# Performance work log

Hardware: AMD Instinct MI355X
Metric: run time of the kernel (lower is better)

Reference implementation:

```python
import jax, jax.numpy as jnp
import numpy as np

CH_IN, CH_OUT, KH, KW = 64, 128, 3, 3


def setup_inputs() -> dict:
    key = jax.random.key(0)
    k1, k2, k3 = jax.random.split(key, 3)
    x = jax.random.normal(k1, (16, CH_IN, 256, 256), dtype=jnp.float32)
    W_hat = jax.random.normal(k2, (CH_OUT, CH_IN * KH * KW), dtype=jnp.float32)
    M_hat = jax.random.normal(k3, (CH_OUT, CH_IN * KH * KW), dtype=jnp.float32)
    return {"x": x, "W_hat": W_hat, "M_hat": M_hat}


def reference(x, W_hat, M_hat):
    # NAC weight transform, then a standard same-padded conv (no bias).
    # Patch flattening order in the original (narrow(-1)/narrow(-2) then reshape)
    # matches (C_in, KH, KW) conv weight layout.
    W = jnp.tanh(W_hat) * jax.nn.sigmoid(M_hat)          # [C_out, C_in*KH*KW]
    W = W.reshape(CH_OUT, CH_IN, KH, KW)                  # OIHW
    out = jax.lax.conv_general_dilated(
        x, W,
        window_strides=(1, 1),
        padding=((KH // 2, KH // 2), (KW // 2, KW // 2)),
        dimension_numbers=("NCHW", "OIHW", "NCHW"),
    )
    return out
```

## Files before the change

### kernel.cpp

```cpp
#include <hip/hip_runtime.h>
#include <hip/hip_bf16.h>
#include <stdint.h>


#define CH_IN  64
#define CH_OUT 128
#define HW     256

typedef __attribute__((ext_vector_type(8))) short short8;
typedef __attribute__((ext_vector_type(4))) float f32x4;

#define AF_BYTES 147456u
#define ZP_BYTE  147456u
#define XB_BYTE  147712u
#define WS_NEED  (147712ull + 134217728ull)

static __device__ __forceinline__ uint32_t pack_bf16(float a, float b) {
    uint32_t ua = __builtin_bit_cast(uint32_t, a);
    uint32_t ub = __builtin_bit_cast(uint32_t, b);
    ua = (ua + 0x7FFFu + ((ua >> 16) & 1u)) >> 16;
    ub = (ub + 0x7FFFu + ((ub >> 16) & 1u));
    return (ua & 0xFFFFu) | (ub & 0xFFFF0000u);
}

__global__ void __launch_bounds__(256) nac_prep(const float* __restrict__ Wh,
                                                const float* __restrict__ Mh,
                                                uint32_t* __restrict__ ws32) {
    if (blockIdx.x == 0 && threadIdx.x < 64) ws32[ZP_BYTE / 4 + threadIdx.x] = 0;

    int f = blockIdx.x * 256 + threadIdx.x;
    if (f >= 9 * 8 * 2 * 64) return;
    int lane = f & 63;
    int s    = (f >> 6) & 1;
    int ms   = (f >> 7) & 7;
    int t    = f >> 10;
    int co   = ms * 16 + (lane & 15);
    int ci0  = s * 32 + ((lane >> 4) << 3);

    uint32_t pk[4];
#pragma unroll
    for (int j2 = 0; j2 < 4; ++j2) {
        int ci = ci0 + 2 * j2;
        int k0 = ci * 9 + t;
        int k1 = k0 + 9;
        float w0 = tanhf(Wh[co * 576 + k0]);
        float m0 = Mh[co * 576 + k0];
        float w1 = tanhf(Wh[co * 576 + k1]);
        float m1 = Mh[co * 576 + k1];
        float v0 = w0 * (1.0f / (1.0f + expf(-m0)));
        float v1 = w1 * (1.0f / (1.0f + expf(-m1)));
        pk[j2] = pack_bf16(v0, v1);
    }
    int fragidx = ((t * 8 + ms) * 2 + s) * 64 + lane;
    reinterpret_cast<uint4*>(ws32)[fragidx] = make_uint4(pk[0], pk[1], pk[2], pk[3]);
}

__global__ void __launch_bounds__(256) nac_convert(const float* __restrict__ x,
                                                   uint32_t* __restrict__ xb) {
    int bid = blockIdx.x;
    int h   = bid & 255;
    int n   = bid >> 8;
    int px  = threadIdx.x;
    const float* xr = x + ((size_t)n * CH_IN * HW + h) * HW + px;
    uint32_t* orow = xb + ((size_t)(n * HW + h) * HW + px) * 32;
#pragma unroll
    for (int g = 0; g < 8; ++g) {
        float v0 = xr[(size_t)(g * 8 + 0) * HW * HW];
        float v1 = xr[(size_t)(g * 8 + 1) * HW * HW];
        float v2 = xr[(size_t)(g * 8 + 2) * HW * HW];
        float v3 = xr[(size_t)(g * 8 + 3) * HW * HW];
        float v4 = xr[(size_t)(g * 8 + 4) * HW * HW];
        float v5 = xr[(size_t)(g * 8 + 5) * HW * HW];
        float v6 = xr[(size_t)(g * 8 + 6) * HW * HW];
        float v7 = xr[(size_t)(g * 8 + 7) * HW * HW];
        uint4 wd;
        wd.x = pack_bf16(v0, v1); wd.y = pack_bf16(v2, v3);
        wd.z = pack_bf16(v4, v5); wd.w = pack_bf16(v6, v7);
        *reinterpret_cast<uint4*>(orow + g * 4) = wd;
    }
}

__global__ void __launch_bounds__(256)
nac_conv2(const uint32_t* __restrict__ xb, const uint32_t* __restrict__ Af,
          float* __restrict__ out, const uint32_t* __restrict__ zp) {
    __shared__ __align__(1024) uint32_t xl[2112 * 4];

    unsigned bid = blockIdx.x;
    unsigned idx = (bid & 7u) * 1024u + (bid >> 3);
    int ht = idx & 127;
    int wt = (idx >> 7) & 3;
    int n  = idx >> 9;
    int h0 = ht * 2;
    int w0 = wt * 64;

    int tid = threadIdx.x;
    int g   = tid & 7;
    int q   = tid >> 3;

#pragma unroll
    for (int it = 0; it < 9; ++it) {
        if (it < 8 || tid < 64) {
            const int rp = it * 32 + q;
            const int r0 = (it * 32) / 66;
            const int r  = (rp >= (r0 + 1) * 66) ? r0 + 1 : r0;
            const int p  = rp - r * 66;
            const int hh = h0 - 1 + r;
            const int ww = w0 - 1 + p;
            const bool valid = ((unsigned)hh < 256u) & ((unsigned)ww < 256u);
            const uint32_t* src = valid
                ? xb + ((size_t)((n * 256 + hh) * 256 + ww) * 32 + ((g ^ (p & 7)) << 2))
                : zp;
            __builtin_amdgcn_global_load_lds(
                (const __attribute__((address_space(1))) uint32_t*)src,
                (__attribute__((address_space(3))) uint32_t*)&xl[(it * 256 + (tid & ~63)) * 4],
                16, 0, 0);
        }
    }
    __syncthreads();

    int lane = tid & 63;
    int wv   = tid >> 6;
    int wm   = wv >> 1;
    int wn   = wv & 1;
    int col  = lane & 15;
    int row4 = lane >> 4;

    int bcol[2][3];
#pragma unroll
    for (int s = 0; s < 2; ++s)
#pragma unroll
        for (int kw = 0; kw < 3; ++kw)
            bcol[s][kw] = (col + kw) * 128 +
                          ((((s * 4) + row4) ^ ((col + kw) & 7)) * 16);

    f32x4 acc[4][4];
#pragma unroll
    for (int mi = 0; mi < 4; ++mi)
#pragma unroll
        for (int ni = 0; ni < 4; ++ni) acc[mi][ni] = (f32x4){0.f, 0.f, 0.f, 0.f};

    const short8* Afr = reinterpret_cast<const short8*>(Af);
    const char* lb = reinterpret_cast<const char*>(xl);

#pragma unroll
    for (int t = 0; t < 9; ++t) {
        const int kh = t / 3, kw = t % 3;
        short8 a[2][4];
#pragma unroll
        for (int s = 0; s < 2; ++s)
#pragma unroll
            for (int mi = 0; mi < 4; ++mi)
                a[s][mi] = Afr[((t * 8 + (wm * 4 + mi)) * 2 + s) * 64 + lane];
#pragma unroll
        for (int s = 0; s < 2; ++s) {
#pragma unroll
            for (int ni = 0; ni < 4; ++ni) {
                short8 b = *reinterpret_cast<const short8*>(
                    lb + ((wn + kh) * 66 + ni * 16) * 128 + bcol[s][kw]);
#pragma unroll
                for (int mi = 0; mi < 4; ++mi)
                    acc[mi][ni] = __builtin_amdgcn_mfma_f32_16x16x32_bf16(
                        a[s][mi], b, acc[mi][ni], 0, 0, 0);
            }
        }
    }

#pragma unroll
    for (int mi = 0; mi < 4; ++mi) {
#pragma unroll
        for (int reg = 0; reg < 4; ++reg) {
            int co = wm * 64 + mi * 16 + row4 * 4 + reg;
            float* op = out + (((size_t)n * CH_OUT + co) * HW + (h0 + wn)) * HW + w0;
#pragma unroll
            for (int ni = 0; ni < 4; ++ni) op[ni * 16 + col] = acc[mi][ni][reg];
        }
    }
}

__global__ void __launch_bounds__(256) nac_conv_fb(const float* __restrict__ x,
                                                   const uint32_t* __restrict__ Af,
                                                   float* __restrict__ out) {
    __shared__ uint32_t xl[8 * 272 * 4];

    unsigned bid = blockIdx.x;
    unsigned idx = (bid & 7u) * 1024u + (bid >> 3);
    int ht = idx & 127;
    int wt = (idx >> 7) & 3;
    int n  = idx >> 9;
    int h0 = ht * 2;
    int w0 = wt * 64;
    int tid = threadIdx.x;

    const float* xn = x + (size_t)n * CH_IN * HW * HW;
    for (int it = 0; it < 9; ++it) {
        int task = tid + it * 256;
        if (task < 2176) {
            int r   = task / 544;
            int rem = task - r * 544;
            int pg  = rem / 68;
            int c   = rem - pg * 68;
            int hrow = h0 - 1 + r;
            int w    = w0 - 1 + c;
            float v[8];
            if ((unsigned)hrow < 256u && (unsigned)w < 256u) {
                const float* p = xn + ((size_t)(pg * 8) * HW + hrow) * HW + w;
#pragma unroll
                for (int e = 0; e < 8; ++e) v[e] = p[(size_t)e * HW * HW];
            } else {
#pragma unroll
                for (int e = 0; e < 8; ++e) v[e] = 0.0f;
            }
            uint4 wd;
            wd.x = pack_bf16(v[0], v[1]);
            wd.y = pack_bf16(v[2], v[3]);
            wd.z = pack_bf16(v[4], v[5]);
            wd.w = pack_bf16(v[6], v[7]);
            *reinterpret_cast<uint4*>(&xl[(pg * 272 + r * 68 + c) * 4]) = wd;
        }
    }
    __syncthreads();

    int lane = tid & 63;
    int wv   = tid >> 6;
    int wm   = wv >> 1;
    int wn   = wv & 1;
    int row4 = lane >> 4;
    int col  = lane & 15;

    f32x4 acc[4][4];
#pragma unroll
    for (int mi = 0; mi < 4; ++mi)
#pragma unroll
        for (int ni = 0; ni < 4; ++ni) acc[mi][ni] = (f32x4){0.f, 0.f, 0.f, 0.f};

    const short8* Afr = reinterpret_cast<const short8*>(Af);
    for (int t = 0; t < 9; ++t) {
        int kh = t / 3, kw = t % 3;
        short8 a[2][4];
#pragma unroll
        for (int s = 0; s < 2; ++s)
#pragma unroll
            for (int mi = 0; mi < 4; ++mi)
                a[s][mi] = Afr[((t * 8 + (wm * 4 + mi)) * 2 + s) * 64 + lane];
#pragma unroll
        for (int s = 0; s < 2; ++s) {
            short8 b[4];
#pragma unroll
            for (int ni = 0; ni < 4; ++ni) {
                int pg = s * 4 + row4;
                int pp = (wn + kh) * 68 + ni * 16 + col + kw;
                b[ni] = *reinterpret_cast<const short8*>(&xl[(pg * 272 + pp) * 4]);
            }
#pragma unroll
            for (int mi = 0; mi < 4; ++mi)
#pragma unroll
                for (int ni = 0; ni < 4; ++ni)
                    acc[mi][ni] = __builtin_amdgcn_mfma_f32_16x16x32_bf16(
                        a[s][mi], b[ni], acc[mi][ni], 0, 0, 0);
        }
    }

#pragma unroll
    for (int mi = 0; mi < 4; ++mi) {
#pragma unroll
        for (int reg = 0; reg < 4; ++reg) {
            int co = wm * 64 + mi * 16 + row4 * 4 + reg;
            float* op = out + (((size_t)n * CH_OUT + co) * HW + (h0 + wn)) * HW + w0;
#pragma unroll
            for (int ni = 0; ni < 4; ++ni) op[ni * 16 + col] = acc[mi][ni][reg];
        }
    }
}

extern "C" void kernel_launch(void* const* d_in, const int* in_sizes, int n_in,
                              void* d_out, int out_size, void* d_ws, size_t ws_size,
                              hipStream_t stream) {
    const float* x  = (const float*)d_in[0];
    const float* Wh = (const float*)d_in[1];
    const float* Mh = (const float*)d_in[2];
    float* out = (float*)d_out;
    uint32_t* ws32 = (uint32_t*)d_ws;
    const uint32_t* Af = ws32;
    const uint32_t* zp = ws32 + ZP_BYTE / 4;
    uint32_t* xb = ws32 + XB_BYTE / 4;

    nac_prep<<<36, 256, 0, stream>>>(Wh, Mh, ws32);
    if (ws_size >= WS_NEED) {
        nac_convert<<<4096, 256, 0, stream>>>(x, xb);
        nac_conv2<<<8192, 256, 0, stream>>>(xb, Af, out, zp);
    } else {
        nac_conv_fb<<<8192, 256, 0, stream>>>(x, Af, out);
    }
}
```

Measured before the change: 376.7 us.

## Tile conv over 16 rows with ring-buffered LDS halo and LDS-resident weights

The conv kernel now gives each block 16 output rows and half of the output channels, down from 2 rows and all channels, so the grid shrinks from 8192 to 2048 blocks. Input rows stream through a 10-slot LDS ring buffer, loading 4 new rows per chunk while the current 4 rows are computed. This reuses halo rows across chunks instead of reloading them per block. The block's half of the weights is staged into LDS once rather than read from global memory on every tap. The cost is about 158KB of LDS per block, which limits occupancy, plus extra pipeline complexity and halo-column special cases.

New measurement: 325.8 us. -13.5%, faster.

```diff
diff --git a/kernel.cpp b/kernel.cpp
--- a/kernel.cpp
+++ b/kernel.cpp
@@ -10,10 +10,14 @@
 typedef __attribute__((ext_vector_type(8))) short short8;
 typedef __attribute__((ext_vector_type(4))) float f32x4;
 
-#define AF_BYTES 147456u
 #define ZP_BYTE  147456u
 #define XB_BYTE  147712u
 #define WS_NEED  (147712ull + 134217728ull)
+
+#define RING_B   81920
+#define HALO_B   2560
+#define ABASE_B  84480
+#define LDS_U32  39552
 
 static __device__ __forceinline__ uint32_t pack_bf16(float a, float b) {
     uint32_t ua = __builtin_bit_cast(uint32_t, a);
@@ -23,9 +27,9 @@
     return (ua & 0xFFFFu) | (ub & 0xFFFF0000u);
 }
 
-__global__ void __launch_bounds__(256) nac_prep(const float* __restrict__ Wh,
-                                                const float* __restrict__ Mh,
-                                                uint32_t* __restrict__ ws32) {
+__global__ void __launch_bounds__(256) nac_prep16(const float* __restrict__ Wh,
+                                                  const float* __restrict__ Mh,
+                                                  uint32_t* __restrict__ ws32) {
     if (blockIdx.x == 0 && threadIdx.x < 64) ws32[ZP_BYTE / 4 + threadIdx.x] = 0;
 
     int f = blockIdx.x * 256 + threadIdx.x;
@@ -81,99 +85,214 @@
 }
 
 __global__ void __launch_bounds__(256)
-nac_conv2(const uint32_t* __restrict__ xb, const uint32_t* __restrict__ Af,
+nac_conv3(const uint32_t* __restrict__ xb, const uint32_t* __restrict__ Af,
           float* __restrict__ out, const uint32_t* __restrict__ zp) {
-    __shared__ __align__(1024) uint32_t xl[2112 * 4];
+    __shared__ __align__(1024) uint32_t lds[LDS_U32];
 
     unsigned bid = blockIdx.x;
-    unsigned idx = (bid & 7u) * 1024u + (bid >> 3);
-    int ht = idx & 127;
-    int wt = (idx >> 7) & 3;
-    int n  = idx >> 9;
-    int h0 = ht * 2;
-    int w0 = wt * 64;
-
-    int tid = threadIdx.x;
-    int g   = tid & 7;
-    int q   = tid >> 3;
-
-#pragma unroll
-    for (int it = 0; it < 9; ++it) {
-        if (it < 8 || tid < 64) {
-            const int rp = it * 32 + q;
-            const int r0 = (it * 32) / 66;
-            const int r  = (rp >= (r0 + 1) * 66) ? r0 + 1 : r0;
-            const int p  = rp - r * 66;
-            const int hh = h0 - 1 + r;
-            const int ww = w0 - 1 + p;
-            const bool valid = ((unsigned)hh < 256u) & ((unsigned)ww < 256u);
-            const uint32_t* src = valid
-                ? xb + ((size_t)((n * 256 + hh) * 256 + ww) * 32 + ((g ^ (p & 7)) << 2))
+    unsigned idx = (bid & 7u) * 256u + (bid >> 3);
+    const int cosplit = idx & 1;
+    const int ht = (idx >> 1) & 15;
+    const int wt = (idx >> 5) & 3;
+    const int n  = idx >> 7;
+    const int h0 = ht * 16, w0 = wt * 64;
+
+    const int tid  = threadIdx.x;
+    const int lane = tid & 63;
+    const int wv   = tid >> 6;
+    const int col  = lane & 15;
+    const int row4 = lane >> 4;
+
+    const char* xbn = reinterpret_cast<const char*>(xb) + ((size_t)n << 23);
+    char* lb = reinterpret_cast<char*>(lds);
+
+#pragma unroll
+    for (int i = 0; i < 18; ++i) {
+        const int fa = i * 4 + wv;
+        const int t  = fa >> 3;
+        const int r8 = fa & 7;
+        const int mi = r8 >> 1;
+        const int s  = r8 & 1;
+        const int gfrag = (t * 8 + cosplit * 4 + mi) * 2 + s;
+        const uint32_t* src = Af + (size_t)(gfrag * 64 + lane) * 4;
+        __builtin_amdgcn_global_load_lds(
+            (const __attribute__((address_space(1))) uint32_t*)src,
+            (__attribute__((address_space(3))) uint32_t*)
+                (lds + (ABASE_B + (i * 256 + (tid & ~63)) * 16) / 4),
+            16, 0, 0);
+    }
+
+    auto stage4 = [&](int slotbase, int hhbase) {
+#pragma unroll
+        for (int i = 0; i < 8; ++i) {
+            const int row = i >> 1;
+            const int jr  = (i & 1) * 256 + tid;
+            const int px  = jr >> 3;
+            const int g   = jr & 7;
+            int sl = slotbase + row; if (sl >= 10) sl -= 10;
+            const int hh = hhbase + row;
+            const int ww = w0 - 1 + px;
+            const bool v = ((unsigned)hh < 256u) & ((unsigned)ww < 256u);
+            const int hhc = v ? hh : 0;
+            const int wwc = v ? ww : 0;
+            const uint32_t* src = v
+                ? (const uint32_t*)(xbn + ((size_t)(hhc * 256 + wwc) << 7)
+                                        + ((g ^ (px & 7)) << 4))
                 : zp;
             __builtin_amdgcn_global_load_lds(
                 (const __attribute__((address_space(1))) uint32_t*)src,
-                (__attribute__((address_space(3))) uint32_t*)&xl[(it * 256 + (tid & ~63)) * 4],
+                (__attribute__((address_space(3))) uint32_t*)
+                    (lds + (sl * 8192 + ((i & 1) * 256 + (tid & ~63)) * 16) / 4),
                 16, 0, 0);
         }
+    };
+
+    stage4(0, h0 - 1);
+#pragma unroll
+    for (int i = 0; i < 4; ++i) {
+        const int row = i >> 1;
+        const int jr  = (i & 1) * 256 + tid;
+        const int px  = jr >> 3;
+        const int g   = jr & 7;
+        const int sl  = 4 + row;
+        const int hh  = h0 + 3 + row;
+        const int ww  = w0 - 1 + px;
+        const bool v  = ((unsigned)hh < 256u) & ((unsigned)ww < 256u);
+        const int hhc = v ? hh : 0;
+        const int wwc = v ? ww : 0;
+        const uint32_t* src = v
+            ? (const uint32_t*)(xbn + ((size_t)(hhc * 256 + wwc) << 7)
+                                    + ((g ^ (px & 7)) << 4))
+            : zp;
+        __builtin_amdgcn_global_load_lds(
+            (const __attribute__((address_space(1))) uint32_t*)src,
+            (__attribute__((address_space(3))) uint32_t*)
+                (lds + (sl * 8192 + ((i & 1) * 256 + (tid & ~63)) * 16) / 4),
+            16, 0, 0);
+    }
+    if (tid < 96) {
+        const int row = tid >> 4;
+        const int hx  = tid & 15;
+        const int px  = 64 + (hx >> 3);
+        const int g   = hx & 7;
+        const int hh  = h0 - 1 + row;
+        const int ww  = w0 - 1 + px;
+        const bool v  = ((unsigned)hh < 256u) & ((unsigned)ww < 256u);
+        const uint32_t* src = v
+            ? (const uint32_t*)(xbn + ((size_t)(hh * 256 + ww) << 7)
+                                    + ((g ^ (px & 7)) << 4))
+            : zp;
+        uint4 hv = *reinterpret_cast<const uint4*>(src);
+        *reinterpret_cast<uint4*>(lb + RING_B + row * 256 + hx * 16) = hv;
     }
     __syncthreads();
 
-    int lane = tid & 63;
-    int wv   = tid >> 6;
-    int wm   = wv >> 1;
-    int wn   = wv & 1;
-    int col  = lane & 15;
-    int row4 = lane >> 4;
-
-    int bcol[2][3];
+    int base[2][3];
+    bool sel3[3];
 #pragma unroll
     for (int s = 0; s < 2; ++s)
 #pragma unroll
-        for (int kw = 0; kw < 3; ++kw)
-            bcol[s][kw] = (col + kw) * 128 +
-                          ((((s * 4) + row4) ^ ((col + kw) & 7)) * 16);
-
-    f32x4 acc[4][4];
-#pragma unroll
-    for (int mi = 0; mi < 4; ++mi)
-#pragma unroll
-        for (int ni = 0; ni < 4; ++ni) acc[mi][ni] = (f32x4){0.f, 0.f, 0.f, 0.f};
-
-    const short8* Afr = reinterpret_cast<const short8*>(Af);
-    const char* lb = reinterpret_cast<const char*>(xl);
-
-#pragma unroll
-    for (int t = 0; t < 9; ++t) {
-        const int kh = t / 3, kw = t % 3;
-        short8 a[2][4];
-#pragma unroll
-        for (int s = 0; s < 2; ++s)
-#pragma unroll
-            for (int mi = 0; mi < 4; ++mi)
-                a[s][mi] = Afr[((t * 8 + (wm * 4 + mi)) * 2 + s) * 64 + lane];
-#pragma unroll
-        for (int s = 0; s < 2; ++s) {
-#pragma unroll
-            for (int ni = 0; ni < 4; ++ni) {
-                short8 b = *reinterpret_cast<const short8*>(
-                    lb + ((wn + kh) * 66 + ni * 16) * 128 + bcol[s][kw]);
-#pragma unroll
-                for (int mi = 0; mi < 4; ++mi)
-                    acc[mi][ni] = __builtin_amdgcn_mfma_f32_16x16x32_bf16(
-                        a[s][mi], b, acc[mi][ni], 0, 0, 0);
+        for (int kw = 0; kw < 3; ++kw) {
+            const int p = col + kw;
+            base[s][kw] = p * 128 + (((s * 4 + row4) ^ (p & 7)) << 4);
+        }
+#pragma unroll
+    for (int kw = 0; kw < 3; ++kw) sel3[kw] = (48 + col + kw) < 64;
+
+    int slR = 0, sstW = 6;
+    for (int c = 0; c < 4; ++c) {
+        const bool st = (c < 3);
+        uint4 hv;
+
+        if (st) {
+            stage4(sstW, h0 + 4 * c + 5);
+            if (tid < 64) {
+                const int row = tid >> 4;
+                const int hx  = tid & 15;
+                const int px  = 64 + (hx >> 3);
+                const int g   = hx & 7;
+                const int hh  = h0 + 4 * c + 5 + row;
+                const int ww  = w0 - 1 + px;
+                const bool v  = ((unsigned)hh < 256u) & ((unsigned)ww < 256u);
+                const uint32_t* src = v
+                    ? (const uint32_t*)(xbn + ((size_t)(hh * 256 + ww) << 7)
+                                            + ((g ^ (px & 7)) << 4))
+                    : zp;
+                hv = *reinterpret_cast<const uint4*>(src);
             }
-        }
-    }
-
-#pragma unroll
-    for (int mi = 0; mi < 4; ++mi) {
-#pragma unroll
-        for (int reg = 0; reg < 4; ++reg) {
-            int co = wm * 64 + mi * 16 + row4 * 4 + reg;
-            float* op = out + (((size_t)n * CH_OUT + co) * HW + (h0 + wn)) * HW + w0;
-#pragma unroll
-            for (int ni = 0; ni < 4; ++ni) op[ni * 16 + col] = acc[mi][ni][reg];
-        }
+            __builtin_amdgcn_sched_barrier(0);
+        }
+
+        f32x4 acc[4][4];
+#pragma unroll
+        for (int mi = 0; mi < 4; ++mi)
+#pragma unroll
+            for (int ni = 0; ni < 4; ++ni) acc[mi][ni] = (f32x4){0.f, 0.f, 0.f, 0.f};
+
+        const int sb = slR + wv;
+#pragma unroll
+        for (int kh = 0; kh < 3; ++kh) {
+            int sl = sb + kh; if (sl >= 10) sl -= 10;
+            const int mb = sl * 8192;
+            const int hb = RING_B + sl * 256;
+#pragma unroll
+            for (int kw = 0; kw < 3; ++kw) {
+                const int t = kh * 3 + kw;
+                const int csel = sel3[kw] ? (mb + 6144) : (hb - 2048);
+#pragma unroll
+                for (int s = 0; s < 2; ++s) {
+                    const int ab = ABASE_B + (t * 8 + s) * 1024 + lane * 16;
+                    short8 a0 = *reinterpret_cast<const short8*>(lb + ab);
+                    short8 a1 = *reinterpret_cast<const short8*>(lb + ab + 2048);
+                    short8 a2 = *reinterpret_cast<const short8*>(lb + ab + 4096);
+                    short8 a3 = *reinterpret_cast<const short8*>(lb + ab + 6144);
+                    const int bb = mb + base[s][kw];
+                    short8 b0 = *reinterpret_cast<const short8*>(lb + bb);
+                    short8 b1 = *reinterpret_cast<const short8*>(lb + bb + 2048);
+                    short8 b2 = *reinterpret_cast<const short8*>(lb + bb + 4096);
+                    short8 b3 = *reinterpret_cast<const short8*>(lb + csel + base[s][kw]);
+                    acc[0][0] = __builtin_amdgcn_mfma_f32_16x16x32_bf16(a0, b0, acc[0][0], 0, 0, 0);
+                    acc[1][0] = __builtin_amdgcn_mfma_f32_16x16x32_bf16(a1, b0, acc[1][0], 0, 0, 0);
+                    acc[2][0] = __builtin_amdgcn_mfma_f32_16x16x32_bf16(a2, b0, acc[2][0], 0, 0, 0);
+                    acc[3][0] = __builtin_amdgcn_mfma_f32_16x16x32_bf16(a3, b0, acc[3][0], 0, 0, 0);
+                    acc[0][1] = __builtin_amdgcn_mfma_f32_16x16x32_bf16(a0, b1, acc[0][1], 0, 0, 0);
+                    acc[1][1] = __builtin_amdgcn_mfma_f32_16x16x32_bf16(a1, b1, acc[1][1], 0, 0, 0);
+                    acc[2][1] = __builtin_amdgcn_mfma_f32_16x16x32_bf16(a2, b1, acc[2][1], 0, 0, 0);
+                    acc[3][1] = __builtin_amdgcn_mfma_f32_16x16x32_bf16(a3, b1, acc[3][1], 0, 0, 0);
+                    acc[0][2] = __builtin_amdgcn_mfma_f32_16x16x32_bf16(a0, b2, acc[0][2], 0, 0, 0);
+                    acc[1][2] = __builtin_amdgcn_mfma_f32_16x16x32_bf16(a1, b2, acc[1][2], 0, 0, 0);
+                    acc[2][2] = __builtin_amdgcn_mfma_f32_16x16x32_bf16(a2, b2, acc[2][2], 0, 0, 0);
+                    acc[3][2] = __builtin_amdgcn_mfma_f32_16x16x32_bf16(a3, b2, acc[3][2], 0, 0, 0);
+                    acc[0][3] = __builtin_amdgcn_mfma_f32_16x16x32_bf16(a0, b3, acc[0][3], 0, 0, 0);
+                    acc[1][3] = __builtin_amdgcn_mfma_f32_16x16x32_bf16(a1, b3, acc[1][3], 0, 0, 0);
+                    acc[2][3] = __builtin_amdgcn_mfma_f32_16x16x32_bf16(a2, b3, acc[2][3], 0, 0, 0);
+                    acc[3][3] = __builtin_amdgcn_mfma_f32_16x16x32_bf16(a3, b3, acc[3][3], 0, 0, 0);
+                }
+            }
+        }
+
+        if (st && tid < 64) {
+            const int row = tid >> 4;
+            const int hx  = tid & 15;
+            int sl = sstW + row; if (sl >= 10) sl -= 10;
+            *reinterpret_cast<uint4*>(lb + RING_B + sl * 256 + hx * 16) = hv;
+        }
+        __syncthreads();
+
+        const int rr = h0 + 4 * c + wv;
+        const size_t ob = (size_t)n * CH_OUT * 65536 + (size_t)rr * 256 + w0;
+#pragma unroll
+        for (int mi = 0; mi < 4; ++mi)
+#pragma unroll
+            for (int reg = 0; reg < 4; ++reg) {
+                const int co = cosplit * 64 + mi * 16 + row4 * 4 + reg;
+                float* op = out + ob + (size_t)co * 65536;
+#pragma unroll
+                for (int ni = 0; ni < 4; ++ni) op[ni * 16 + col] = acc[mi][ni][reg];
+            }
+
+        slR += 4;  if (slR >= 10)  slR -= 10;
+        sstW += 4; if (sstW >= 10) sstW -= 10;
     }
 }
 
@@ -181,7 +300,6 @@
                                                    const uint32_t* __restrict__ Af,
                                                    float* __restrict__ out) {
     __shared__ uint32_t xl[8 * 272 * 4];
-
     unsigned bid = blockIdx.x;
     unsigned idx = (bid & 7u) * 1024u + (bid >> 3);
     int ht = idx & 127;
@@ -282,12 +400,12 @@
     uint32_t* ws32 = (uint32_t*)d_ws;
     const uint32_t* Af = ws32;
     const uint32_t* zp = ws32 + ZP_BYTE / 4;
-    uint32_t* xb = ws32 + XB_BYTE / 4;
-
-    nac_prep<<<36, 256, 0, stream>>>(Wh, Mh, ws32);
+    uint32_t* xbuf = ws32 + XB_BYTE / 4;
+
+    nac_prep16<<<36, 256, 0, stream>>>(Wh, Mh, ws32);
     if (ws_size >= WS_NEED) {
-        nac_convert<<<4096, 256, 0, stream>>>(x, xb);
-        nac_conv2<<<8192, 256, 0, stream>>>(xb, Af, out, zp);
+        nac_convert<<<4096, 256, 0, stream>>>(x, xbuf);
+        nac_conv3<<<2048, 256, 0, stream>>>(xbuf, Af, out, zp);
     } else {
         nac_conv_fb<<<8192, 256, 0, stream>>>(x, Af, out);
     }
```

## Process 16 output rows per block with a ring buffer of staged input rows

Applied to the files above, without the earlier changes.

Each block now covers 16 output rows instead of 2, using 512 threads. Input rows are staged into a 10-slot LDS ring buffer, and the next 4 rows are prefetched while the current 4 are computed. This cuts the redundant halo reloads of the bf16 input, which were about double the input, down to about 1.1x, and overlaps loads with MFMA work. In exchange the grid has fewer, larger blocks with more LDS each, and the correctness of the async LDS loads depends on the barrier placement.

Result: slower. 618.4 us (+64.1%).

```diff
diff --git a/kernel.cpp b/kernel.cpp
--- a/kernel.cpp
+++ b/kernel.cpp
@@ -10,10 +10,12 @@
 typedef __attribute__((ext_vector_type(8))) short short8;
 typedef __attribute__((ext_vector_type(4))) float f32x4;
 
-#define AF_BYTES 147456u
 #define ZP_BYTE  147456u
 #define XB_BYTE  147712u
 #define WS_NEED  (147712ull + 134217728ull)
+
+#define NSLOT   10
+#define SLOT_B  8448
 
 static __device__ __forceinline__ uint32_t pack_bf16(float a, float b) {
     uint32_t ua = __builtin_bit_cast(uint32_t, a);
@@ -23,9 +25,9 @@
     return (ua & 0xFFFFu) | (ub & 0xFFFF0000u);
 }
 
-__global__ void __launch_bounds__(256) nac_prep(const float* __restrict__ Wh,
-                                                const float* __restrict__ Mh,
-                                                uint32_t* __restrict__ ws32) {
+__global__ void __launch_bounds__(256) nac_prep16(const float* __restrict__ Wh,
+                                                  const float* __restrict__ Mh,
+                                                  uint32_t* __restrict__ ws32) {
     if (blockIdx.x == 0 && threadIdx.x < 64) ws32[ZP_BYTE / 4 + threadIdx.x] = 0;
 
     int f = blockIdx.x * 256 + threadIdx.x;
@@ -80,100 +82,134 @@
     }
 }
 
-__global__ void __launch_bounds__(256)
-nac_conv2(const uint32_t* __restrict__ xb, const uint32_t* __restrict__ Af,
+__global__ void __launch_bounds__(512, 2)
+nac_conv4(const uint32_t* __restrict__ xb, const uint32_t* __restrict__ Af,
           float* __restrict__ out, const uint32_t* __restrict__ zp) {
-    __shared__ __align__(1024) uint32_t xl[2112 * 4];
+    __shared__ __align__(1024) uint32_t xl[NSLOT * SLOT_B / 4];
 
     unsigned bid = blockIdx.x;
-    unsigned idx = (bid & 7u) * 1024u + (bid >> 3);
-    int ht = idx & 127;
-    int wt = (idx >> 7) & 3;
-    int n  = idx >> 9;
-    int h0 = ht * 2;
-    int w0 = wt * 64;
-
-    int tid = threadIdx.x;
-    int g   = tid & 7;
-    int q   = tid >> 3;
-
-#pragma unroll
-    for (int it = 0; it < 9; ++it) {
-        if (it < 8 || tid < 64) {
-            const int rp = it * 32 + q;
-            const int r0 = (it * 32) / 66;
-            const int r  = (rp >= (r0 + 1) * 66) ? r0 + 1 : r0;
-            const int p  = rp - r * 66;
-            const int hh = h0 - 1 + r;
-            const int ww = w0 - 1 + p;
-            const bool valid = ((unsigned)hh < 256u) & ((unsigned)ww < 256u);
-            const uint32_t* src = valid
-                ? xb + ((size_t)((n * 256 + hh) * 256 + ww) * 32 + ((g ^ (p & 7)) << 2))
+    unsigned idx = (bid & 7u) * 128u + (bid >> 3);
+    const int ht = idx & 15;
+    const int wt = (idx >> 4) & 3;
+    const int n  = idx >> 6;
+    const int h0 = ht * 16, w0 = wt * 64;
+
+    const int tid  = threadIdx.x;
+    const int lane = tid & 63;
+    const int wv   = tid >> 6;
+    const int wm   = wv >> 2;
+    const int wn   = wv & 3;
+    const int col  = lane & 15;
+    const int row4 = lane >> 4;
+
+    const char* xbn = reinterpret_cast<const char*>(xb) + ((size_t)n << 23);
+    const char* lb  = reinterpret_cast<const char*>(xl);
+
+    auto stage_row = [&](int slot, int hh) {
+#pragma unroll
+        for (int off = 0; off <= 16; off += 16) {
+            const int jr = off + tid;
+            const int px = jr >> 3;
+            const int g  = jr & 7;
+            const int ww = w0 - 1 + px;
+            const bool v = ((unsigned)hh < 256u) & ((unsigned)ww < 256u);
+            const int hc = v ? hh : 0;
+            const int wc = v ? ww : 0;
+            const uint32_t* src = v
+                ? (const uint32_t*)(xbn + ((size_t)(hc * 256 + wc) << 7)
+                                        + ((g ^ (px & 7)) << 4))
                 : zp;
             __builtin_amdgcn_global_load_lds(
                 (const __attribute__((address_space(1))) uint32_t*)src,
-                (__attribute__((address_space(3))) uint32_t*)&xl[(it * 256 + (tid & ~63)) * 4],
+                (__attribute__((address_space(3))) uint32_t*)
+                    (xl + (slot * SLOT_B + (off + (tid & ~63)) * 16) / 4),
                 16, 0, 0);
         }
-    }
+    };
+
+#pragma unroll
+    for (int L = 0; L < 6; ++L) stage_row(L, h0 - 1 + L);
     __syncthreads();
 
-    int lane = tid & 63;
-    int wv   = tid >> 6;
-    int wm   = wv >> 1;
-    int wn   = wv & 1;
-    int col  = lane & 15;
-    int row4 = lane >> 4;
-
-    int bcol[2][3];
+    int boff[2][3];
 #pragma unroll
     for (int s = 0; s < 2; ++s)
 #pragma unroll
-        for (int kw = 0; kw < 3; ++kw)
-            bcol[s][kw] = (col + kw) * 128 +
-                          ((((s * 4) + row4) ^ ((col + kw) & 7)) * 16);
-
-    f32x4 acc[4][4];
-#pragma unroll
-    for (int mi = 0; mi < 4; ++mi)
-#pragma unroll
-        for (int ni = 0; ni < 4; ++ni) acc[mi][ni] = (f32x4){0.f, 0.f, 0.f, 0.f};
+        for (int kw = 0; kw < 3; ++kw) {
+            const int p = col + kw;
+            boff[s][kw] = p * 128 + (((s * 4 + row4) ^ (p & 7)) << 4);
+        }
 
     const short8* Afr = reinterpret_cast<const short8*>(Af);
-    const char* lb = reinterpret_cast<const char*>(xl);
-
-#pragma unroll
-    for (int t = 0; t < 9; ++t) {
-        const int kh = t / 3, kw = t % 3;
-        short8 a[2][4];
-#pragma unroll
-        for (int s = 0; s < 2; ++s)
-#pragma unroll
-            for (int mi = 0; mi < 4; ++mi)
-                a[s][mi] = Afr[((t * 8 + (wm * 4 + mi)) * 2 + s) * 64 + lane];
-#pragma unroll
-        for (int s = 0; s < 2; ++s) {
-#pragma unroll
-            for (int ni = 0; ni < 4; ++ni) {
-                short8 b = *reinterpret_cast<const short8*>(
-                    lb + ((wn + kh) * 66 + ni * 16) * 128 + bcol[s][kw]);
-#pragma unroll
-                for (int mi = 0; mi < 4; ++mi)
-                    acc[mi][ni] = __builtin_amdgcn_mfma_f32_16x16x32_bf16(
-                        a[s][mi], b, acc[mi][ni], 0, 0, 0);
-            }
-        }
-    }
-
-#pragma unroll
-    for (int mi = 0; mi < 4; ++mi) {
-#pragma unroll
-        for (int reg = 0; reg < 4; ++reg) {
-            int co = wm * 64 + mi * 16 + row4 * 4 + reg;
-            float* op = out + (((size_t)n * CH_OUT + co) * HW + (h0 + wn)) * HW + w0;
-#pragma unroll
-            for (int ni = 0; ni < 4; ++ni) op[ni * 16 + col] = acc[mi][ni][reg];
-        }
+
+    for (int c = 0; c < 4; ++c) {
+        if (c < 3) {
+#pragma unroll
+            for (int r = 0; r < 4; ++r) {
+                int sl = 4 * c + 6 + r; if (sl >= NSLOT) sl -= NSLOT;
+                stage_row(sl, h0 + 4 * c + 5 + r);
+            }
+        }
+
+        f32x4 acc[4][4];
+#pragma unroll
+        for (int mi = 0; mi < 4; ++mi)
+#pragma unroll
+            for (int ni = 0; ni < 4; ++ni) acc[mi][ni] = (f32x4){0.f, 0.f, 0.f, 0.f};
+
+        int sb = 4 * c + wn; if (sb >= NSLOT) sb -= NSLOT;
+#pragma unroll
+        for (int kh = 0; kh < 3; ++kh) {
+            int sl = sb + kh; if (sl >= NSLOT) sl -= NSLOT;
+            const int mb = sl * SLOT_B;
+#pragma unroll
+            for (int kw = 0; kw < 3; ++kw) {
+                const int t = kh * 3 + kw;
+#pragma unroll
+                for (int s = 0; s < 2; ++s) {
+                    const int abase = ((t * 8 + wm * 4) * 2 + s) * 64 + lane;
+                    short8 a0 = Afr[abase];
+                    short8 a1 = Afr[abase + 128];
+                    short8 a2 = Afr[abase + 256];
+                    short8 a3 = Afr[abase + 384];
+                    const char* bp = lb + mb + boff[s][kw];
+                    short8 b0 = *reinterpret_cast<const short8*>(bp);
+                    short8 b1 = *reinterpret_cast<const short8*>(bp + 2048);
+                    short8 b2 = *reinterpret_cast<const short8*>(bp + 4096);
+                    short8 b3 = *reinterpret_cast<const short8*>(bp + 6144);
+                    acc[0][0] = __builtin_amdgcn_mfma_f32_16x16x32_bf16(a0, b0, acc[0][0], 0, 0, 0);
+                    acc[1][0] = __builtin_amdgcn_mfma_f32_16x16x32_bf16(a1, b0, acc[1][0], 0, 0, 0);
+                    acc[2][0] = __builtin_amdgcn_mfma_f32_16x16x32_bf16(a2, b0, acc[2][0], 0, 0, 0);
+                    acc[3][0] = __builtin_amdgcn_mfma_f32_16x16x32_bf16(a3, b0, acc[3][0], 0, 0, 0);
+                    acc[0][1] = __builtin_amdgcn_mfma_f32_16x16x32_bf16(a0, b1, acc[0][1], 0, 0, 0);
+                    acc[1][1] = __builtin_amdgcn_mfma_f32_16x16x32_bf16(a1, b1, acc[1][1], 0, 0, 0);
+                    acc[2][1] = __builtin_amdgcn_mfma_f32_16x16x32_bf16(a2, b1, acc[2][1], 0, 0, 0);
+                    acc[3][1] = __builtin_amdgcn_mfma_f32_16x16x32_bf16(a3, b1, acc[3][1], 0, 0, 0);
+                    acc[0][2] = __builtin_amdgcn_mfma_f32_16x16x32_bf16(a0, b2, acc[0][2], 0, 0, 0);
+                    acc[1][2] = __builtin_amdgcn_mfma_f32_16x16x32_bf16(a1, b2, acc[1][2], 0, 0, 0);
+                    acc[2][2] = __builtin_amdgcn_mfma_f32_16x16x32_bf16(a2, b2, acc[2][2], 0, 0, 0);
+                    acc[3][2] = __builtin_amdgcn_mfma_f32_16x16x32_bf16(a3, b2, acc[3][2], 0, 0, 0);
+                    acc[0][3] = __builtin_amdgcn_mfma_f32_16x16x32_bf16(a0, b3, acc[0][3], 0, 0, 0);
+                    acc[1][3] = __builtin_amdgcn_mfma_f32_16x16x32_bf16(a1, b3, acc[1][3], 0, 0, 0);
+                    acc[2][3] = __builtin_amdgcn_mfma_f32_16x16x32_bf16(a2, b3, acc[2][3], 0, 0, 0);
+                    acc[3][3] = __builtin_amdgcn_mfma_f32_16x16x32_bf16(a3, b3, acc[3][3], 0, 0, 0);
+                }
+            }
+        }
+
+        __syncthreads();
+
+        const int rr = h0 + 4 * c + wn;
+        const size_t ob = (size_t)n * CH_OUT * 65536 + (size_t)rr * 256 + w0;
+#pragma unroll
+        for (int mi = 0; mi < 4; ++mi)
+#pragma unroll
+            for (int reg = 0; reg < 4; ++reg) {
+                const int co = wm * 64 + mi * 16 + row4 * 4 + reg;
+                float* op = out + ob + (size_t)co * 65536;
+#pragma unroll
+                for (int ni = 0; ni < 4; ++ni) op[ni * 16 + col] = acc[mi][ni][reg];
+            }
     }
 }
 
@@ -181,7 +217,6 @@
                                                    const uint32_t* __restrict__ Af,
                                                    float* __restrict__ out) {
     __shared__ uint32_t xl[8 * 272 * 4];
-
     unsigned bid = blockIdx.x;
     unsigned idx = (bid & 7u) * 1024u + (bid >> 3);
     int ht = idx & 127;
@@ -282,12 +317,12 @@
     uint32_t* ws32 = (uint32_t*)d_ws;
     const uint32_t* Af = ws32;
     const uint32_t* zp = ws32 + ZP_BYTE / 4;
-    uint32_t* xb = ws32 + XB_BYTE / 4;
-
-    nac_prep<<<36, 256, 0, stream>>>(Wh, Mh, ws32);
+    uint32_t* xbuf = ws32 + XB_BYTE / 4;
+
+    nac_prep16<<<36, 256, 0, stream>>>(Wh, Mh, ws32);
     if (ws_size >= WS_NEED) {
-        nac_convert<<<4096, 256, 0, stream>>>(x, xb);
-        nac_conv2<<<8192, 256, 0, stream>>>(xb, Af, out, zp);
+        nac_convert<<<4096, 256, 0, stream>>>(x, xbuf);
+        nac_conv4<<<1024, 512, 0, stream>>>(xbuf, Af, out, zp);
     } else {
         nac_conv_fb<<<8192, 256, 0, stream>>>(x, Af, out);
     }
```
